# Performance work log

Measured on AMD Instinct MI355X. Metric: run time of the kernel, lower is better.

The kernel has to match this reference:

```python
import jax, jax.numpy as jnp
import numpy as np

VOCAB = 50000
OOV = 100
UNITS = 512
EMB = UNITS // 2
N_SENT = 32
N_WORDS = 50
B = 64


def setup_inputs() -> dict:
    key = jax.random.key(0)
    ks = jax.random.split(key, 16)
    g = lambda k, sh, s=0.02: (jax.random.normal(k, sh, dtype=jnp.float32) * s)
    inp = {
        "embedded_target": jax.random.normal(ks[0], (B, 1, EMB), dtype=jnp.float32),
        "hidden_dec": jax.random.normal(ks[1], (B, UNITS), dtype=jnp.float32),
        "encoded_sentences": jax.random.normal(ks[2], (B, N_SENT, UNITS), dtype=jnp.float32),
        "encoded_words": jax.random.normal(ks[3], (B, N_SENT, N_WORDS, UNITS), dtype=jnp.float32),
        "numeric_input": jax.random.randint(ks[4], (B, N_SENT * N_WORDS), 0, VOCAB + OOV),
        "batch_size": B,
        # GRU params (keras reset_after=True layout: 3 gates z,r,h stacked)
        "gru_Wx": g(ks[5], (EMB, 3 * UNITS)),
        "gru_Wh": g(ks[6], (UNITS, 3 * UNITS)),
        "gru_b": jnp.zeros((2, 3 * UNITS), dtype=jnp.float32),
        # attention params
        "W_att_sent": g(ks[7], (UNITS, UNITS)),
        "W_att_word": g(ks[8], (UNITS, UNITS)),
        # output projection (input is dec_units//2 after weight_dec)
        "fc_W": g(ks[9], (UNITS // 2, VOCAB)),
        "fc_b": jnp.zeros((VOCAB,), dtype=jnp.float32),
        "weight_context": g(ks[10], (UNITS, 1)),
        "weight_hidden": g(ks[11], (UNITS, 1)),
        "weight_dec": g(ks[12], (2 * UNITS, UNITS // 2)),
        "weight_input": g(ks[13], (UNITS // 2, 1)),
    }
    return inp


def _gru_step(x, h, Wx, Wh, b):
    # keras GRU cell, reset_after=True
    xm = x @ Wx + b[0]            # [B, 3U]
    hm = h @ Wh + b[1]            # [B, 3U]
    xz, xr, xh = jnp.split(xm, 3, axis=-1)
    hz, hr, hh = jnp.split(hm, 3, axis=-1)
    z = jax.nn.sigmoid(xz + hz)
    r = jax.nn.sigmoid(xr + hr)
    hcand = jnp.tanh(xh + r * hh)
    return z * h + (1.0 - z) * hcand


def reference(embedded_target, hidden_dec, encoded_sentences, encoded_words,
              gru_Wx, gru_Wh, gru_b, W_att_sent, W_att_word, fc_W, fc_b,
              weight_context, weight_hidden, weight_dec, weight_input,
              numeric_input, batch_size):
    # ---- GRU over the (length-1) target step; return last hidden ----
    def step(h, x_t):
        h2 = _gru_step(x_t, h, gru_Wx, gru_Wh, gru_b)
        return h2, None
    dec_output, _ = jax.lax.scan(step, hidden_dec, jnp.swapaxes(embedded_target, 0, 1))

    # ---- Luong (general) attention over sentences ----
    q = dec_output @ W_att_sent                              # [B, U]
    score_s = jnp.einsum("bd,bsd->bs", q, encoded_sentences)  # [B, S]
    alpha = jax.nn.softmax(score_s, axis=-1)                  # [B, S]
    context = jnp.einsum("bs,bsd->bd", alpha, encoded_sentences)  # [B, U]

    # ---- generation distribution ----
    x = jnp.concatenate([context, dec_output], axis=-1)       # [B, 2U]
    hidden_t = jnp.tanh(x @ weight_dec)                       # [B, U/2]
    gen_distr = jax.nn.softmax(hidden_t @ fc_W + fc_b, axis=-1)
    gen_distr = jnp.pad(gen_distr, ((0, 0), (0, OOV)))        # [B, V+OOV]

    # ---- hierarchical word attention (word softmax per sentence, scaled by alpha) ----
    qw = dec_output @ W_att_word                              # [B, U]
    score_w = jnp.einsum("bd,bswd->bsw", qw, encoded_words)   # [B, S, W]
    word_attn = jax.nn.softmax(score_w, axis=-1)              # softmax over words
    beta = (alpha[:, :, None] * word_attn).reshape(batch_size, -1)  # [B, S*W]

    # ---- batched scatter-add copy distribution ----
    ext = VOCAB + OOV
    bidx = jnp.arange(batch_size)[:, None]
    copy_distr = jnp.zeros((batch_size, ext), dtype=beta.dtype).at[bidx, numeric_input].add(beta)

    # ---- generation gate ----
    res1 = context @ weight_context
    res2 = dec_output @ weight_hidden
    res3 = embedded_target.reshape(batch_size, EMB) @ weight_input
    p_gen = jax.nn.sigmoid(res1 + res2 + res3)                # [B, 1]

    return dec_output, gen_distr, copy_distr, p_gen
```

## Files before the change

### kernel.cpp

```cpp
#include <hip/hip_runtime.h>

#define VOCAB 50000
#define OOV   100
#define EXT   50100
#define UNITS 512
#define EMB   256
#define NS    32
#define NW    50
#define BATCH 64
#define NQ    8
#define BINS_PER ((EXT + NQ - 1) / NQ)

#define GKC   24
#define QKC   8
#define HKC   16
#define NCB   ((VOCAB + 63) / 64)

#define COPYB (NQ * BATCH)
#define FINB  ((BATCH * (EXT / 4) + 255) / 256)

using short8 = __attribute__((ext_vector_type(8))) short;
using f32x4  = __attribute__((ext_vector_type(4))) float;

__device__ __forceinline__ float sigmoidf_(float x) { return 1.f / (1.f + __expf(-x)); }

__device__ __forceinline__ unsigned short f2bf_(float x) {
  union { float f; unsigned u; } c; c.f = x;
  return (unsigned short)((c.u + 0x8000u) >> 16);
}

__device__ __forceinline__ void gload_lds16(const void* g, void* l) {
  __builtin_amdgcn_global_load_lds(
      (const __attribute__((address_space(1))) unsigned int*)g,
      (__attribute__((address_space(3))) unsigned int*)l, 16, 0, 0);
}

__global__ __launch_bounds__(256) void k_gru_part(
    const float* __restrict__ emb, const float* __restrict__ h0,
    const float* __restrict__ Wx, const float* __restrict__ Wh,
    float* __restrict__ gates)
{
  __shared__ float sv[32];
  const int kc = blockIdx.x, b = blockIdx.y, t = threadIdx.x, u0 = 2 * t;
  const int base = kc * 32;
  const bool isx = base < EMB;
  if (t < 32) sv[t] = isx ? emb[b * EMB + base + t] : h0[b * UNITS + base - EMB + t];
  __syncthreads();

  const float* W = isx ? (Wx + (size_t)base * 1536) : (Wh + (size_t)(base - EMB) * 1536);
  float azx = 0.f, azy = 0.f, arx = 0.f, ary = 0.f, ahx = 0.f, ahy = 0.f;
  for (int i = 0; i < 32; i += 4) {
    float2 wz[4], wr[4], wh[4];
#pragma unroll
    for (int j = 0; j < 4; ++j) {
      const float* row = W + (size_t)(i + j) * 1536;
      wz[j] = *(const float2*)(row + u0);
      wr[j] = *(const float2*)(row + 512 + u0);
      wh[j] = *(const float2*)(row + 1024 + u0);
    }
#pragma unroll
    for (int j = 0; j < 4; ++j) {
      const float v = sv[i + j];
      azx = fmaf(v, wz[j].x, azx); azy = fmaf(v, wz[j].y, azy);
      arx = fmaf(v, wr[j].x, arx); ary = fmaf(v, wr[j].y, ary);
      ahx = fmaf(v, wh[j].x, ahx); ahy = fmaf(v, wh[j].y, ahy);
    }
  }
  float* gb_ = gates + (size_t)b * 2048;
  atomicAdd(gb_ + u0, azx);           atomicAdd(gb_ + u0 + 1, azy);
  atomicAdd(gb_ + 512 + u0, arx);     atomicAdd(gb_ + 512 + u0 + 1, ary);
  const int ho = isx ? 1024 : 1536;
  atomicAdd(gb_ + ho + u0, ahx);      atomicAdd(gb_ + ho + u0 + 1, ahy);
}

__global__ __launch_bounds__(256) void k_gru_fin(
    const float* __restrict__ gates, const float* __restrict__ gb,
    const float* __restrict__ h0, const float* __restrict__ emb,
    const float* __restrict__ whid, const float* __restrict__ winp,
    float* __restrict__ ws_dec, float* __restrict__ out_dec,
    float* __restrict__ ws_pgen)
{
  __shared__ float sred[256];
  const int b = blockIdx.x, t = threadIdx.x, u0 = 2 * t;
  const float* g_ = gates + (size_t)b * 2048;
  const float2 az  = *(const float2*)(g_ + u0);
  const float2 ar  = *(const float2*)(g_ + 512 + u0);
  const float2 ahx = *(const float2*)(g_ + 1024 + u0);
  const float2 ahh = *(const float2*)(g_ + 1536 + u0);

  const float2 b0z = *(const float2*)(gb + u0);
  const float2 b0r = *(const float2*)(gb + 512 + u0);
  const float2 b0h = *(const float2*)(gb + 1024 + u0);
  const float2 b1z = *(const float2*)(gb + 1536 + u0);
  const float2 b1r = *(const float2*)(gb + 1536 + 512 + u0);
  const float2 b1h = *(const float2*)(gb + 1536 + 1024 + u0);
  const float2 hp  = *(const float2*)(h0 + b * UNITS + u0);

  const float z0 = sigmoidf_(az.x + b0z.x + b1z.x);
  const float z1 = sigmoidf_(az.y + b0z.y + b1z.y);
  const float r0 = sigmoidf_(ar.x + b0r.x + b1r.x);
  const float r1 = sigmoidf_(ar.y + b0r.y + b1r.y);
  const float c0 = tanhf(ahx.x + b0h.x + r0 * (ahh.x + b1h.x));
  const float c1 = tanhf(ahx.y + b0h.y + r1 * (ahh.y + b1h.y));
  const float n0 = z0 * hp.x + (1.f - z0) * c0;
  const float n1 = z1 * hp.y + (1.f - z1) * c1;
  ws_dec[b * UNITS + u0]      = n0;
  ws_dec[b * UNITS + u0 + 1]  = n1;
  out_dec[b * UNITS + u0]     = n0;
  out_dec[b * UNITS + u0 + 1] = n1;

  float p = n0 * whid[u0] + n1 * whid[u0 + 1];
  if (u0 < EMB) p += emb[b * EMB + u0] * winp[u0] + emb[b * EMB + u0 + 1] * winp[u0 + 1];
  sred[t] = p;
  __syncthreads();
  for (int off = 128; off > 0; off >>= 1) {
    if (t < off) sred[t] += sred[t + off];
    __syncthreads();
  }
  if (t == 0) atomicAdd(ws_pgen + b, sred[0]);
}

__global__ __launch_bounds__(256) void k_qq(
    const float* __restrict__ ws_dec, const float* __restrict__ Wsent,
    const float* __restrict__ Wword, float* __restrict__ qsum)
{
  __shared__ float sdec[64];
  const int kc = blockIdx.x, b = blockIdx.y, t = threadIdx.x, u0 = 2 * t;
  const int k0 = kc * 64;
  if (t < 64) sdec[t] = ws_dec[b * UNITS + k0 + t];
  __syncthreads();

  float qx = 0.f, qy = 0.f, wx = 0.f, wy = 0.f;
  for (int i = 0; i < 64; i += 4) {
    float2 a[4], c[4];
#pragma unroll
    for (int j = 0; j < 4; ++j) {
      a[j] = *(const float2*)(Wsent + (size_t)(k0 + i + j) * UNITS + u0);
      c[j] = *(const float2*)(Wword + (size_t)(k0 + i + j) * UNITS + u0);
    }
#pragma unroll
    for (int j = 0; j < 4; ++j) {
      const float d = sdec[i + j];
      qx = fmaf(d, a[j].x, qx); qy = fmaf(d, a[j].y, qy);
      wx = fmaf(d, c[j].x, wx); wy = fmaf(d, c[j].y, wy);
    }
  }
  float* o = qsum + (size_t)b * 1024;
  atomicAdd(o + u0, qx);           atomicAdd(o + u0 + 1, qy);
  atomicAdd(o + 512 + u0, wx);     atomicAdd(o + 512 + u0 + 1, wy);
}

__global__ __launch_bounds__(512) void k_attn(
    const float* __restrict__ qsum, const float* __restrict__ encS,
    const float* __restrict__ wctx, float* __restrict__ ws_alpha,
    float* __restrict__ ctxsum, float* __restrict__ ws_pgen)
{
  __shared__ float sq[UNITS];
  __shared__ float sscore[NS];
  __shared__ float salpha[NS];
  __shared__ float sred[512];
  const int b = blockIdx.x, t = threadIdx.x;
  sq[t] = qsum[(size_t)b * 1024 + t];
  __syncthreads();

  const int wave = t >> 6, lane = t & 63;
  float qr[8];
#pragma unroll
  for (int j = 0; j < 8; ++j) qr[j] = sq[lane * 8 + j];
  for (int s = wave; s < NS; s += 8) {
    const float* base = encS + ((size_t)(b * NS + s)) * UNITS + lane * 8;
    const float4 v0 = *(const float4*)(base);
    const float4 v1 = *(const float4*)(base + 4);
    float acc = 0.f;
    acc = fmaf(v0.x, qr[0], acc); acc = fmaf(v0.y, qr[1], acc);
    acc = fmaf(v0.z, qr[2], acc); acc = fmaf(v0.w, qr[3], acc);
    acc = fmaf(v1.x, qr[4], acc); acc = fmaf(v1.y, qr[5], acc);
    acc = fmaf(v1.z, qr[6], acc); acc = fmaf(v1.w, qr[7], acc);
#pragma unroll
    for (int off = 32; off > 0; off >>= 1) acc += __shfl_down(acc, off);
    if (lane == 0) sscore[s] = acc;
  }
  __syncthreads();

  if (t < 32) {
    const float v = sscore[t];
    float m = v;
#pragma unroll
    for (int off = 16; off > 0; off >>= 1) m = fmaxf(m, __shfl_xor(m, off));
    const float e = __expf(v - m);
    float ssum = e;
#pragma unroll
    for (int off = 16; off > 0; off >>= 1) ssum += __shfl_xor(ssum, off);
    const float a = e / ssum;
    salpha[t] = a;
    ws_alpha[b * NS + t] = a;
  }
  __syncthreads();

  float c = 0.f;
#pragma unroll 4
  for (int s = 0; s < NS; ++s)
    c = fmaf(salpha[s], encS[((size_t)(b * NS + s)) * UNITS + t], c);
  ctxsum[b * UNITS + t] = c;

  float p = c * wctx[t];
  sred[t] = p;
  __syncthreads();
  for (int off = 256; off > 0; off >>= 1) {
    if (t < off) sred[t] += sred[t + off];
    __syncthreads();
  }
  if (t == 0) atomicAdd(ws_pgen + b, sred[0]);
}

__global__ __launch_bounds__(128) void k_ht(
    const float* __restrict__ ctxsum, const float* __restrict__ ws_dec,
    const float* __restrict__ wdec, float* __restrict__ htsum)
{
  __shared__ float scat[64];
  const int kc = blockIdx.x, b = blockIdx.y, t = threadIdx.x, u0 = 2 * t;
  const int k0 = kc * 64;
  if (t < 64) {
    const int k = k0 + t;
    scat[t] = (k < UNITS) ? ctxsum[b * UNITS + k] : ws_dec[b * UNITS + k - UNITS];
  }
  __syncthreads();

  float ax = 0.f, ay = 0.f;
  for (int i = 0; i < 64; i += 8) {
    float2 w[8];
#pragma unroll
    for (int j = 0; j < 8; ++j)
      w[j] = *(const float2*)(wdec + (size_t)(k0 + i + j) * 256 + u0);
#pragma unroll
    for (int j = 0; j < 8; ++j) {
      const float v = scat[i + j];
      ax = fmaf(v, w[j].x, ax); ay = fmaf(v, w[j].y, ay);
    }
  }
  atomicAdd(htsum + b * EMB + u0, ax);
  atomicAdd(htsum + b * EMB + u0 + 1, ay);
}

__global__ __launch_bounds__(256) void k_ht_fin(
    const float* __restrict__ htsum, const float* __restrict__ ws_pgen,
    unsigned short* __restrict__ Af, float* __restrict__ out_pgen)
{
  const int rb = blockIdx.x, t = threadIdx.x, l = t & 63, kh = t >> 6;
  const int row = rb * 16 + (l & 15);
#pragma unroll
  for (int ks = kh; ks < 8; ks += 4) {
    const int k0 = ks * 32 + (l >> 4) * 8;
    const float4 h0 = *(const float4*)(htsum + row * EMB + k0);
    const float4 h1 = *(const float4*)(htsum + row * EMB + k0 + 4);
    short8 v;
    v[0] = (short)f2bf_(tanhf(h0.x)); v[1] = (short)f2bf_(tanhf(h0.y));
    v[2] = (short)f2bf_(tanhf(h0.z)); v[3] = (short)f2bf_(tanhf(h0.w));
    v[4] = (short)f2bf_(tanhf(h1.x)); v[5] = (short)f2bf_(tanhf(h1.y));
    v[6] = (short)f2bf_(tanhf(h1.z)); v[7] = (short)f2bf_(tanhf(h1.w));
    *(short8*)(Af + ((size_t)(rb * 8 + ks)) * 512 + l * 8) = v;
  }
  if (rb == 0 && t < BATCH) out_pgen[t] = sigmoidf_(ws_pgen[t]);
}

__global__ __launch_bounds__(256, 2) void k_fc(
    const unsigned short* __restrict__ Af, const float* __restrict__ fcW,
    const float* __restrict__ fcb, float* __restrict__ out_gen,
    float* __restrict__ ws_rowsum)
{
  __shared__ float swt[256 * 64];
  const int cb = blockIdx.x;
  const int t = threadIdx.x, rb = t >> 6, l = t & 63;

  {
    const int c4 = l & 15;
    const int gc = cb * 64 + c4 * 4;
    const bool oob = (gc >= VOCAB);
    const int kr = rb * 64 + (l >> 4);
#pragma unroll
    for (int q = 0; q < 16; ++q) {
      const float* src = oob ? (fcW + c4 * 4)
                             : (fcW + (size_t)(kr + q * 4) * VOCAB + gc);
      gload_lds16(src, swt + rb * 4096 + q * 256);
    }
  }

  short8 a[8];
#pragma unroll
  for (int ks = 0; ks < 8; ++ks)
    a[ks] = *(const short8*)(Af + ((size_t)(rb * 8 + ks)) * 512 + l * 8);

  __syncthreads();

  f32x4 acc0 = {0.f, 0.f, 0.f, 0.f};
  f32x4 acc1 = {0.f, 0.f, 0.f, 0.f};
  f32x4 acc2 = {0.f, 0.f, 0.f, 0.f};
  f32x4 acc3 = {0.f, 0.f, 0.f, 0.f};

  const int cr = l & 15;
  const int kb = (l >> 4) * 8;
#pragma unroll
  for (int ks = 0; ks < 8; ++ks) {
    const float* kbase = swt + (size_t)(ks * 32 + kb) * 64 + cr;
    short8 b0, b1, b2, b3;
#pragma unroll
    for (int j = 0; j < 8; ++j) {
      const float* rowp = kbase + j * 64;
      b0[j] = (short)f2bf_(rowp[0]);
      b1[j] = (short)f2bf_(rowp[16]);
      b2[j] = (short)f2bf_(rowp[32]);
      b3[j] = (short)f2bf_(rowp[48]);
    }
    acc0 = __builtin_amdgcn_mfma_f32_16x16x32_bf16(a[ks], b0, acc0, 0, 0, 0);
    acc1 = __builtin_amdgcn_mfma_f32_16x16x32_bf16(a[ks], b1, acc1, 0, 0, 0);
    acc2 = __builtin_amdgcn_mfma_f32_16x16x32_bf16(a[ks], b2, acc2, 0, 0, 0);
    acc3 = __builtin_amdgcn_mfma_f32_16x16x32_bf16(a[ks], b3, acc3, 0, 0, 0);
  }

  const int colbase = cb * 64 + (l & 15);
  const int rowbase = rb * 16 + (l >> 4) * 4;
#pragma unroll
  for (int p = 0; p < 4; ++p) {
    float rs = 0.f;
    const float av[4] = {acc0[p], acc1[p], acc2[p], acc3[p]};
#pragma unroll
    for (int f = 0; f < 4; ++f) {
      const int col = colbase + f * 16;
      if (col < VOCAB) {
        const float e = __expf(av[f] + fcb[col]);
        out_gen[(size_t)(rowbase + p) * EXT + col] = e;
        rs += e;
      }
    }
    rs += __shfl_xor(rs, 1); rs += __shfl_xor(rs, 2);
    rs += __shfl_xor(rs, 4); rs += __shfl_xor(rs, 8);
    if ((l & 15) == 0) atomicAdd(ws_rowsum + rowbase + p, rs);
  }
}

__global__ __launch_bounds__(256) void k_word(
    const float* __restrict__ qsum, const float* __restrict__ encW,
    const float* __restrict__ ws_alpha, float* __restrict__ ws_beta)
{
  __shared__ float sqw[UNITS];
  __shared__ float sscore[64];
  const int bi = blockIdx.x;
  const int b = bi >> 5, s = bi & 31;
  const int t = threadIdx.x;
  sqw[t]       = qsum[(size_t)b * 1024 + 512 + t];
  sqw[t + 256] = qsum[(size_t)b * 1024 + 768 + t];
  __syncthreads();

  const int wave = t >> 6, lane = t & 63;
  float qr[8];
#pragma unroll
  for (int j = 0; j < 8; ++j) qr[j] = sqw[lane * 8 + j];
  const float* base = encW + ((size_t)(b * NS + s)) * NW * UNITS + lane * 8;

#pragma unroll
  for (int i = 0; i < 4; ++i) {
    const int r0 = i * 16 + wave * 4;
    if (r0 >= NW) break;
    float a0 = 0.f, a1 = 0.f, a2 = 0.f, a3 = 0.f;
    {
      const float* row = base + (size_t)r0 * UNITS;
      const float4 v0 = *(const float4*)(row);
      const float4 v1 = *(const float4*)(row + 4);
      a0 = v0.x*qr[0] + v0.y*qr[1] + v0.z*qr[2] + v0.w*qr[3]
         + v1.x*qr[4] + v1.y*qr[5] + v1.z*qr[6] + v1.w*qr[7];
    }
    if (r0 + 1 < NW) {
      const float* row = base + (size_t)(r0 + 1) * UNITS;
      const float4 v0 = *(const float4*)(row);
      const float4 v1 = *(const float4*)(row + 4);
      a1 = v0.x*qr[0] + v0.y*qr[1] + v0.z*qr[2] + v0.w*qr[3]
         + v1.x*qr[4] + v1.y*qr[5] + v1.z*qr[6] + v1.w*qr[7];
    }
    if (r0 + 2 < NW) {
      const float* row = base + (size_t)(r0 + 2) * UNITS;
      const float4 v0 = *(const float4*)(row);
      const float4 v1 = *(const float4*)(row + 4);
      a2 = v0.x*qr[0] + v0.y*qr[1] + v0.z*qr[2] + v0.w*qr[3]
         + v1.x*qr[4] + v1.y*qr[5] + v1.z*qr[6] + v1.w*qr[7];
    }
    if (r0 + 3 < NW) {
      const float* row = base + (size_t)(r0 + 3) * UNITS;
      const float4 v0 = *(const float4*)(row);
      const float4 v1 = *(const float4*)(row + 4);
      a3 = v0.x*qr[0] + v0.y*qr[1] + v0.z*qr[2] + v0.w*qr[3]
         + v1.x*qr[4] + v1.y*qr[5] + v1.z*qr[6] + v1.w*qr[7];
    }
#pragma unroll
    for (int off = 32; off > 0; off >>= 1) {
      a0 += __shfl_xor(a0, off);
      a1 += __shfl_xor(a1, off);
      a2 += __shfl_xor(a2, off);
      a3 += __shfl_xor(a3, off);
    }
    if (lane == 0) {
      sscore[r0] = a0;
      if (r0 + 1 < NW) sscore[r0 + 1] = a1;
      if (r0 + 2 < NW) sscore[r0 + 2] = a2;
      if (r0 + 3 < NW) sscore[r0 + 3] = a3;
    }
  }
  __syncthreads();

  if (t < 64) {
    const float v = (t < NW) ? sscore[t] : -1e30f;
    float m = v;
#pragma unroll
    for (int off = 32; off > 0; off >>= 1) m = fmaxf(m, __shfl_xor(m, off));
    const float e = (t < NW) ? __expf(v - m) : 0.f;
    float sum = e;
#pragma unroll
    for (int off = 32; off > 0; off >>= 1) sum += __shfl_xor(sum, off);
    if (t < NW)
      ws_beta[b * (NS * NW) + s * NW + t] = ws_alpha[b * NS + s] * e / sum;
  }
}

__global__ __launch_bounds__(256) void k_tail(
    const int* __restrict__ nidx, const float* __restrict__ ws_beta,
    const float* __restrict__ ws_rowsum, float* __restrict__ out_copy,
    float* __restrict__ out_gen)
{
  __shared__ float shist[BINS_PER];
  const int bid = blockIdx.x, t = threadIdx.x;
  if (bid < COPYB) {
    const int q = bid & (NQ - 1), b = bid >> 3;
    const int base = q * BINS_PER;
    const int len = min(BINS_PER, EXT - base);

    for (int j = t; j < BINS_PER; j += 256) shist[j] = 0.f;
    __syncthreads();

    for (int e = t; e < NS * NW; e += 256) {
      const int rel = nidx[b * (NS * NW) + e] - base;
      if (rel >= 0 && rel < len) atomicAdd(shist + rel, ws_beta[b * (NS * NW) + e]);
    }
    __syncthreads();

    for (int j = t; j < len; j += 256)
      out_copy[(size_t)b * EXT + base + j] = shist[j];
  } else {
    const int i4 = (bid - COPYB) * 256 + t;
    if (i4 < BATCH * (EXT / 4)) {
      const int b = i4 / (EXT / 4);
      const int c4 = (i4 - b * (EXT / 4)) * 4;
      float4 v = make_float4(0.f, 0.f, 0.f, 0.f);
      if (c4 < VOCAB) {
        v = *(const float4*)(out_gen + (size_t)b * EXT + c4);
        const float inv = 1.f / ws_rowsum[b];
        v.x *= inv; v.y *= inv; v.z *= inv; v.w *= inv;
      }
      *(float4*)(out_gen + (size_t)b * EXT + c4) = v;
    }
  }
}

extern "C" void kernel_launch(void* const* d_in, const int* in_sizes, int n_in,
                              void* d_out, int out_size, void* d_ws, size_t ws_size,
                              hipStream_t stream)
{
  const float* emb   = (const float*)d_in[0];
  const float* h0    = (const float*)d_in[1];
  const float* encS  = (const float*)d_in[2];
  const float* encW  = (const float*)d_in[3];
  const int*   nidx  = (const int*)d_in[4];
  const float* Wx    = (const float*)d_in[6];
  const float* Wh    = (const float*)d_in[7];
  const float* gb    = (const float*)d_in[8];
  const float* Wsent = (const float*)d_in[9];
  const float* Wword = (const float*)d_in[10];
  const float* fcW   = (const float*)d_in[11];
  const float* fcb   = (const float*)d_in[12];
  const float* wctx  = (const float*)d_in[13];
  const float* whid  = (const float*)d_in[14];
  const float* wdec  = (const float*)d_in[15];
  const float* winp  = (const float*)d_in[16];

  float* ws = (float*)d_ws;
  float* ws_gates  = ws;
  float* ws_qsum   = ws_gates + BATCH * 2048;
  float* ws_ctxsum = ws_qsum + BATCH * 1024;
  float* ws_htsum  = ws_ctxsum + BATCH * UNITS;
  float* ws_rowsum = ws_htsum + BATCH * EMB;
  float* ws_pgen   = ws_rowsum + BATCH;
  const size_t zfloats = (size_t)BATCH * (2048 + 1024 + 512 + 256) + 2 * BATCH;
  float* ws_dec    = ws_pgen + BATCH;
  float* ws_alpha  = ws_dec + BATCH * UNITS;
  float* ws_beta   = ws_alpha + BATCH * NS;
  unsigned short* ws_af = (unsigned short*)(ws_beta + BATCH * NS * NW);

  float* out      = (float*)d_out;
  float* out_dec  = out;
  float* out_gen  = out + BATCH * UNITS;
  float* out_copy = out_gen + (size_t)BATCH * EXT;
  float* out_pgen = out_copy + (size_t)BATCH * EXT;

  hipMemsetAsync(ws, 0, zfloats * sizeof(float), stream);

  k_gru_part<<<dim3(GKC, BATCH), 256, 0, stream>>>(emb, h0, Wx, Wh, ws_gates);
  k_gru_fin<<<BATCH, 256, 0, stream>>>(ws_gates, gb, h0, emb, whid, winp,
                                       ws_dec, out_dec, ws_pgen);
  k_qq<<<dim3(QKC, BATCH), 256, 0, stream>>>(ws_dec, Wsent, Wword, ws_qsum);
  k_attn<<<BATCH, 512, 0, stream>>>(ws_qsum, encS, wctx, ws_alpha,
                                    ws_ctxsum, ws_pgen);
  k_ht<<<dim3(HKC, BATCH), 128, 0, stream>>>(ws_ctxsum, ws_dec, wdec, ws_htsum);
  k_ht_fin<<<4, 256, 0, stream>>>(ws_htsum, ws_pgen, ws_af, out_pgen);
  k_fc<<<NCB, 256, 0, stream>>>(ws_af, fcW, fcb, out_gen, ws_rowsum);
  k_word<<<BATCH * NS, 256, 0, stream>>>(ws_qsum, encW, ws_alpha, ws_beta);
  k_tail<<<COPYB + FINB, 256, 0, stream>>>(nidx, ws_beta, ws_rowsum,
                                           out_copy, out_gen);
}
```

Baseline: 505.0 us.

## Fuse kernel chain with last-block atomic tickets and merge word-attn with fc

Cuts the launch chain from nine kernels to five. Each split-K partial kernel (GRU, q-projection, weight_dec) now takes an atomic ticket per batch or globally, and the last-arriving block performs the finalize step (gate nonlinearity, attention softmax/context, tanh+bf16 pack) that used to be a separate launch. The word-attention blocks and the fc MFMA blocks share one launch, and the fc path stages its weight tile in two halves so it uses 32KB of LDS instead of 64KB, allowing more resident blocks. The aim is to remove launch gaps and tail idle time, at the cost of threadfence and atomic-counter overhead and serial finalize work done by one block.

```diff
diff --git a/kernel.cpp b/kernel.cpp
--- a/kernel.cpp
+++ b/kernel.cpp
@@ -15,6 +15,7 @@
 #define QKC   8
 #define HKC   16
 #define NCB   ((VOCAB + 63) / 64)
+#define WORDB (BATCH * NS)
 
 #define COPYB (NQ * BATCH)
 #define FINB  ((BATCH * (EXT / 4) + 255) / 256)
@@ -35,12 +36,18 @@
       (__attribute__((address_space(3))) unsigned int*)l, 16, 0, 0);
 }
 
-__global__ __launch_bounds__(256) void k_gru_part(
+__global__ __launch_bounds__(256) void k_gru(
     const float* __restrict__ emb, const float* __restrict__ h0,
     const float* __restrict__ Wx, const float* __restrict__ Wh,
-    float* __restrict__ gates)
+    const float* __restrict__ gb, const float* __restrict__ whid,
+    const float* __restrict__ winp,
+    float* __restrict__ gates, float* __restrict__ ws_dec,
+    float* __restrict__ out_dec, float* __restrict__ ws_pgen,
+    unsigned* __restrict__ cnt)
 {
   __shared__ float sv[32];
+  __shared__ float sred[256];
+  __shared__ unsigned sticket;
   const int kc = blockIdx.x, b = blockIdx.y, t = threadIdx.x, u0 = 2 * t;
   const int base = kc * 32;
   const bool isx = base < EMB;
@@ -48,7 +55,7 @@
   __syncthreads();
 
   const float* W = isx ? (Wx + (size_t)base * 1536) : (Wh + (size_t)(base - EMB) * 1536);
-  float azx = 0.f, azy = 0.f, arx = 0.f, ary = 0.f, ahx = 0.f, ahy = 0.f;
+  float azx = 0.f, azy = 0.f, arx = 0.f, ary = 0.f, ahxx = 0.f, ahy = 0.f;
   for (int i = 0; i < 32; i += 4) {
     float2 wz[4], wr[4], wh[4];
 #pragma unroll
@@ -63,25 +70,22 @@
       const float v = sv[i + j];
       azx = fmaf(v, wz[j].x, azx); azy = fmaf(v, wz[j].y, azy);
       arx = fmaf(v, wr[j].x, arx); ary = fmaf(v, wr[j].y, ary);
-      ahx = fmaf(v, wh[j].x, ahx); ahy = fmaf(v, wh[j].y, ahy);
+      ahxx = fmaf(v, wh[j].x, ahxx); ahy = fmaf(v, wh[j].y, ahy);
     }
   }
   float* gb_ = gates + (size_t)b * 2048;
   atomicAdd(gb_ + u0, azx);           atomicAdd(gb_ + u0 + 1, azy);
   atomicAdd(gb_ + 512 + u0, arx);     atomicAdd(gb_ + 512 + u0 + 1, ary);
   const int ho = isx ? 1024 : 1536;
-  atomicAdd(gb_ + ho + u0, ahx);      atomicAdd(gb_ + ho + u0 + 1, ahy);
-}
-
-__global__ __launch_bounds__(256) void k_gru_fin(
-    const float* __restrict__ gates, const float* __restrict__ gb,
-    const float* __restrict__ h0, const float* __restrict__ emb,
-    const float* __restrict__ whid, const float* __restrict__ winp,
-    float* __restrict__ ws_dec, float* __restrict__ out_dec,
-    float* __restrict__ ws_pgen)
-{
-  __shared__ float sred[256];
-  const int b = blockIdx.x, t = threadIdx.x, u0 = 2 * t;
+  atomicAdd(gb_ + ho + u0, ahxx);     atomicAdd(gb_ + ho + u0 + 1, ahy);
+
+  __threadfence();
+  __syncthreads();
+  if (t == 0) sticket = atomicAdd(&cnt[b], 1u);
+  __syncthreads();
+  if (sticket != GKC - 1) return;
+  __threadfence();
+
   const float* g_ = gates + (size_t)b * 2048;
   const float2 az  = *(const float2*)(g_ + u0);
   const float2 ar  = *(const float2*)(g_ + 512 + u0);
@@ -120,11 +124,19 @@
   if (t == 0) atomicAdd(ws_pgen + b, sred[0]);
 }
 
-__global__ __launch_bounds__(256) void k_qq(
+__global__ __launch_bounds__(256) void k_qa(
     const float* __restrict__ ws_dec, const float* __restrict__ Wsent,
-    const float* __restrict__ Wword, float* __restrict__ qsum)
+    const float* __restrict__ Wword, const float* __restrict__ encS,
+    const float* __restrict__ wctx,
+    float* __restrict__ qsum, float* __restrict__ ws_alpha,
+    float* __restrict__ ctxsum, float* __restrict__ ws_pgen,
+    unsigned* __restrict__ cnt)
 {
   __shared__ float sdec[64];
+  __shared__ float sq[UNITS];
+  __shared__ float sscore[NS], salpha[NS];
+  __shared__ float sred[256];
+  __shared__ unsigned sticket;
   const int kc = blockIdx.x, b = blockIdx.y, t = threadIdx.x, u0 = 2 * t;
   const int k0 = kc * 64;
   if (t < 64) sdec[t] = ws_dec[b * UNITS + k0 + t];
@@ -148,26 +160,23 @@
   float* o = qsum + (size_t)b * 1024;
   atomicAdd(o + u0, qx);           atomicAdd(o + u0 + 1, qy);
   atomicAdd(o + 512 + u0, wx);     atomicAdd(o + 512 + u0 + 1, wy);
-}
-
-__global__ __launch_bounds__(512) void k_attn(
-    const float* __restrict__ qsum, const float* __restrict__ encS,
-    const float* __restrict__ wctx, float* __restrict__ ws_alpha,
-    float* __restrict__ ctxsum, float* __restrict__ ws_pgen)
-{
-  __shared__ float sq[UNITS];
-  __shared__ float sscore[NS];
-  __shared__ float salpha[NS];
-  __shared__ float sred[512];
-  const int b = blockIdx.x, t = threadIdx.x;
-  sq[t] = qsum[(size_t)b * 1024 + t];
+
+  __threadfence();
+  __syncthreads();
+  if (t == 0) sticket = atomicAdd(&cnt[b], 1u);
+  __syncthreads();
+  if (sticket != QKC - 1) return;
+  __threadfence();
+
+  sq[t]       = o[t];
+  sq[t + 256] = o[t + 256];
   __syncthreads();
 
   const int wave = t >> 6, lane = t & 63;
   float qr[8];
 #pragma unroll
   for (int j = 0; j < 8; ++j) qr[j] = sq[lane * 8 + j];
-  for (int s = wave; s < NS; s += 8) {
+  for (int s = wave; s < NS; s += 4) {
     const float* base = encS + ((size_t)(b * NS + s)) * UNITS + lane * 8;
     const float4 v0 = *(const float4*)(base);
     const float4 v1 = *(const float4*)(base + 4);
@@ -197,27 +206,33 @@
   }
   __syncthreads();
 
-  float c = 0.f;
+  float c0 = 0.f, c1 = 0.f;
 #pragma unroll 4
-  for (int s = 0; s < NS; ++s)
-    c = fmaf(salpha[s], encS[((size_t)(b * NS + s)) * UNITS + t], c);
-  ctxsum[b * UNITS + t] = c;
-
-  float p = c * wctx[t];
-  sred[t] = p;
-  __syncthreads();
-  for (int off = 256; off > 0; off >>= 1) {
+  for (int s = 0; s < NS; ++s) {
+    const float* es = encS + ((size_t)(b * NS + s)) * UNITS;
+    c0 = fmaf(salpha[s], es[t], c0);
+    c1 = fmaf(salpha[s], es[t + 256], c1);
+  }
+  ctxsum[b * UNITS + t]       = c0;
+  ctxsum[b * UNITS + t + 256] = c1;
+
+  sred[t] = c0 * wctx[t] + c1 * wctx[t + 256];
+  __syncthreads();
+  for (int off = 128; off > 0; off >>= 1) {
     if (t < off) sred[t] += sred[t + off];
     __syncthreads();
   }
   if (t == 0) atomicAdd(ws_pgen + b, sred[0]);
 }
 
-__global__ __launch_bounds__(128) void k_ht(
+__global__ __launch_bounds__(128) void k_hta(
     const float* __restrict__ ctxsum, const float* __restrict__ ws_dec,
-    const float* __restrict__ wdec, float* __restrict__ htsum)
+    const float* __restrict__ wdec, const float* __restrict__ ws_pgen,
+    float* __restrict__ htsum, unsigned short* __restrict__ Af,
+    float* __restrict__ out_pgen, unsigned* __restrict__ cnt)
 {
   __shared__ float scat[64];
+  __shared__ unsigned sticket;
   const int kc = blockIdx.x, b = blockIdx.y, t = threadIdx.x, u0 = 2 * t;
   const int k0 = kc * 64;
   if (t < 64) {
@@ -240,57 +255,129 @@
   }
   atomicAdd(htsum + b * EMB + u0, ax);
   atomicAdd(htsum + b * EMB + u0 + 1, ay);
-}
-
-__global__ __launch_bounds__(256) void k_ht_fin(
-    const float* __restrict__ htsum, const float* __restrict__ ws_pgen,
-    unsigned short* __restrict__ Af, float* __restrict__ out_pgen)
+
+  __threadfence();
+  __syncthreads();
+  if (t == 0) sticket = atomicAdd(cnt, 1u);
+  __syncthreads();
+  if (sticket != HKC * BATCH - 1) return;
+  __threadfence();
+
+  const int l = t & 63, wv = t >> 6;
+#pragma unroll
+  for (int rb = 0; rb < 4; ++rb) {
+    for (int ks = wv; ks < 8; ks += 2) {
+      const int row = rb * 16 + (l & 15);
+      const int kk = ks * 32 + (l >> 4) * 8;
+      const float4 h0v = *(const float4*)(htsum + row * EMB + kk);
+      const float4 h1v = *(const float4*)(htsum + row * EMB + kk + 4);
+      short8 v;
+      v[0] = (short)f2bf_(tanhf(h0v.x)); v[1] = (short)f2bf_(tanhf(h0v.y));
+      v[2] = (short)f2bf_(tanhf(h0v.z)); v[3] = (short)f2bf_(tanhf(h0v.w));
+      v[4] = (short)f2bf_(tanhf(h1v.x)); v[5] = (short)f2bf_(tanhf(h1v.y));
+      v[6] = (short)f2bf_(tanhf(h1v.z)); v[7] = (short)f2bf_(tanhf(h1v.w));
+      *(short8*)(Af + ((size_t)(rb * 8 + ks)) * 512 + l * 8) = v;
+    }
+  }
+  if (t < BATCH) out_pgen[t] = sigmoidf_(ws_pgen[t]);
+}
+
+__global__ __launch_bounds__(256, 5) void k_fw(
+    const unsigned short* __restrict__ Af, const float* __restrict__ fcW,
+    const float* __restrict__ fcb, const float* __restrict__ qsum,
+    const float* __restrict__ encW, const float* __restrict__ ws_alpha,
+    float* __restrict__ out_gen, float* __restrict__ ws_rowsum,
+    float* __restrict__ ws_beta)
 {
-  const int rb = blockIdx.x, t = threadIdx.x, l = t & 63, kh = t >> 6;
-  const int row = rb * 16 + (l & 15);
-#pragma unroll
-  for (int ks = kh; ks < 8; ks += 4) {
-    const int k0 = ks * 32 + (l >> 4) * 8;
-    const float4 h0 = *(const float4*)(htsum + row * EMB + k0);
-    const float4 h1 = *(const float4*)(htsum + row * EMB + k0 + 4);
-    short8 v;
-    v[0] = (short)f2bf_(tanhf(h0.x)); v[1] = (short)f2bf_(tanhf(h0.y));
-    v[2] = (short)f2bf_(tanhf(h0.z)); v[3] = (short)f2bf_(tanhf(h0.w));
-    v[4] = (short)f2bf_(tanhf(h1.x)); v[5] = (short)f2bf_(tanhf(h1.y));
-    v[6] = (short)f2bf_(tanhf(h1.z)); v[7] = (short)f2bf_(tanhf(h1.w));
-    *(short8*)(Af + ((size_t)(rb * 8 + ks)) * 512 + l * 8) = v;
-  }
-  if (rb == 0 && t < BATCH) out_pgen[t] = sigmoidf_(ws_pgen[t]);
-}
-
-__global__ __launch_bounds__(256, 2) void k_fc(
-    const unsigned short* __restrict__ Af, const float* __restrict__ fcW,
-    const float* __restrict__ fcb, float* __restrict__ out_gen,
-    float* __restrict__ ws_rowsum)
-{
-  __shared__ float swt[256 * 64];
-  const int cb = blockIdx.x;
-  const int t = threadIdx.x, rb = t >> 6, l = t & 63;
-
-  {
-    const int c4 = l & 15;
-    const int gc = cb * 64 + c4 * 4;
-    const bool oob = (gc >= VOCAB);
-    const int kr = rb * 64 + (l >> 4);
-#pragma unroll
-    for (int q = 0; q < 16; ++q) {
-      const float* src = oob ? (fcW + c4 * 4)
-                             : (fcW + (size_t)(kr + q * 4) * VOCAB + gc);
-      gload_lds16(src, swt + rb * 4096 + q * 256);
-    }
-  }
+  __shared__ __align__(16) float smem[8192];
+  const int bid = blockIdx.x, t = threadIdx.x;
+
+  if (bid < WORDB) {
+    float* sqw    = smem;
+    float* sscore = smem + 512;
+    const int b = bid >> 5, s = bid & 31;
+    sqw[t]       = qsum[(size_t)b * 1024 + 512 + t];
+    sqw[t + 256] = qsum[(size_t)b * 1024 + 768 + t];
+    __syncthreads();
+
+    const int wave = t >> 6, lane = t & 63;
+    float qr[8];
+#pragma unroll
+    for (int j = 0; j < 8; ++j) qr[j] = sqw[lane * 8 + j];
+    const float* base = encW + ((size_t)(b * NS + s)) * NW * UNITS + lane * 8;
+
+#pragma unroll
+    for (int i = 0; i < 4; ++i) {
+      const int r0 = i * 16 + wave * 4;
+      if (r0 >= NW) break;
+      float a0 = 0.f, a1 = 0.f, a2 = 0.f, a3 = 0.f;
+      {
+        const float* row = base + (size_t)r0 * UNITS;
+        const float4 v0 = *(const float4*)(row);
+        const float4 v1 = *(const float4*)(row + 4);
+        a0 = v0.x*qr[0] + v0.y*qr[1] + v0.z*qr[2] + v0.w*qr[3]
+           + v1.x*qr[4] + v1.y*qr[5] + v1.z*qr[6] + v1.w*qr[7];
+      }
+      if (r0 + 1 < NW) {
+        const float* row = base + (size_t)(r0 + 1) * UNITS;
+        const float4 v0 = *(const float4*)(row);
+        const float4 v1 = *(const float4*)(row + 4);
+        a1 = v0.x*qr[0] + v0.y*qr[1] + v0.z*qr[2] + v0.w*qr[3]
+           + v1.x*qr[4] + v1.y*qr[5] + v1.z*qr[6] + v1.w*qr[7];
+      }
+      if (r0 + 2 < NW) {
+        const float* row = base + (size_t)(r0 + 2) * UNITS;
+        const float4 v0 = *(const float4*)(row);
+        const float4 v1 = *(const float4*)(row + 4);
+        a2 = v0.x*qr[0] + v0.y*qr[1] + v0.z*qr[2] + v0.w*qr[3]
+           + v1.x*qr[4] + v1.y*qr[5] + v1.z*qr[6] + v1.w*qr[7];
+      }
+      if (r0 + 3 < NW) {
+        const float* row = base + (size_t)(r0 + 3) * UNITS;
+        const float4 v0 = *(const float4*)(row);
+        const float4 v1 = *(const float4*)(row + 4);
+        a3 = v0.x*qr[0] + v0.y*qr[1] + v0.z*qr[2] + v0.w*qr[3]
+           + v1.x*qr[4] + v1.y*qr[5] + v1.z*qr[6] + v1.w*qr[7];
+      }
+#pragma unroll
+      for (int off = 32; off > 0; off >>= 1) {
+        a0 += __shfl_xor(a0, off);
+        a1 += __shfl_xor(a1, off);
+        a2 += __shfl_xor(a2, off);
+        a3 += __shfl_xor(a3, off);
+      }
+      if (lane == 0) {
+        sscore[r0] = a0;
+        if (r0 + 1 < NW) sscore[r0 + 1] = a1;
+        if (r0 + 2 < NW) sscore[r0 + 2] = a2;
+        if (r0 + 3 < NW) sscore[r0 + 3] = a3;
+      }
+    }
+    __syncthreads();
+
+    if (t < 64) {
+      const float v = (t < NW) ? sscore[t] : -1e30f;
+      float m = v;
+#pragma unroll
+      for (int off = 32; off > 0; off >>= 1) m = fmaxf(m, __shfl_xor(m, off));
+      const float e = (t < NW) ? __expf(v - m) : 0.f;
+      float sum = e;
+#pragma unroll
+      for (int off = 32; off > 0; off >>= 1) sum += __shfl_xor(sum, off);
+      if (t < NW)
+        ws_beta[b * (NS * NW) + s * NW + t] = ws_alpha[b * NS + s] * e / sum;
+    }
+    return;
+  }
+
+  const int cb = bid - WORDB;
+  float* swt = smem;
+  const int rb = t >> 6, l = t & 63;
 
   short8 a[8];
 #pragma unroll
   for (int ks = 0; ks < 8; ++ks)
     a[ks] = *(const short8*)(Af + ((size_t)(rb * 8 + ks)) * 512 + l * 8);
-
-  __syncthreads();
 
   f32x4 acc0 = {0.f, 0.f, 0.f, 0.f};
   f32x4 acc1 = {0.f, 0.f, 0.f, 0.f};
@@ -299,22 +386,39 @@
 
   const int cr = l & 15;
   const int kb = (l >> 4) * 8;
-#pragma unroll
-  for (int ks = 0; ks < 8; ++ks) {
-    const float* kbase = swt + (size_t)(ks * 32 + kb) * 64 + cr;
-    short8 b0, b1, b2, b3;
-#pragma unroll
-    for (int j = 0; j < 8; ++j) {
-      const float* rowp = kbase + j * 64;
-      b0[j] = (short)f2bf_(rowp[0]);
-      b1[j] = (short)f2bf_(rowp[16]);
-      b2[j] = (short)f2bf_(rowp[32]);
-      b3[j] = (short)f2bf_(rowp[48]);
-    }
-    acc0 = __builtin_amdgcn_mfma_f32_16x16x32_bf16(a[ks], b0, acc0, 0, 0, 0);
-    acc1 = __builtin_amdgcn_mfma_f32_16x16x32_bf16(a[ks], b1, acc1, 0, 0, 0);
-    acc2 = __builtin_amdgcn_mfma_f32_16x16x32_bf16(a[ks], b2, acc2, 0, 0, 0);
-    acc3 = __builtin_amdgcn_mfma_f32_16x16x32_bf16(a[ks], b3, acc3, 0, 0, 0);
+  const int gc = cb * 64 + cr * 4;
+  const bool oob = (gc >= VOCAB);
+
+#pragma unroll
+  for (int h = 0; h < 2; ++h) {
+    if (h) __syncthreads();
+    const int krow0 = h * 128 + rb * 32;
+#pragma unroll
+    for (int q = 0; q < 8; ++q) {
+      const float* src = oob ? (fcW + cr * 4)
+          : (fcW + (size_t)(krow0 + q * 4 + (l >> 4)) * VOCAB + gc);
+      gload_lds16(src, swt + (rb * 32 + q * 4) * 64);
+    }
+    __syncthreads();
+
+#pragma unroll
+    for (int ks2 = 0; ks2 < 4; ++ks2) {
+      const float* kbase = swt + (size_t)(ks2 * 32 + kb) * 64 + cr;
+      short8 b0, b1, b2, b3;
+#pragma unroll
+      for (int j = 0; j < 8; ++j) {
+        const float* rowp = kbase + j * 64;
+        b0[j] = (short)f2bf_(rowp[0]);
+        b1[j] = (short)f2bf_(rowp[16]);
+        b2[j] = (short)f2bf_(rowp[32]);
+        b3[j] = (short)f2bf_(rowp[48]);
+      }
+      const int ks = h * 4 + ks2;
+      acc0 = __builtin_amdgcn_mfma_f32_16x16x32_bf16(a[ks], b0, acc0, 0, 0, 0);
+      acc1 = __builtin_amdgcn_mfma_f32_16x16x32_bf16(a[ks], b1, acc1, 0, 0, 0);
+      acc2 = __builtin_amdgcn_mfma_f32_16x16x32_bf16(a[ks], b2, acc2, 0, 0, 0);
+      acc3 = __builtin_amdgcn_mfma_f32_16x16x32_bf16(a[ks], b3, acc3, 0, 0, 0);
+    }
   }
 
   const int colbase = cb * 64 + (l & 15);
@@ -335,88 +439,6 @@
     rs += __shfl_xor(rs, 1); rs += __shfl_xor(rs, 2);
     rs += __shfl_xor(rs, 4); rs += __shfl_xor(rs, 8);
     if ((l & 15) == 0) atomicAdd(ws_rowsum + rowbase + p, rs);
-  }
-}
-
-__global__ __launch_bounds__(256) void k_word(
-    const float* __restrict__ qsum, const float* __restrict__ encW,
-    const float* __restrict__ ws_alpha, float* __restrict__ ws_beta)
-{
-  __shared__ float sqw[UNITS];
-  __shared__ float sscore[64];
-  const int bi = blockIdx.x;
-  const int b = bi >> 5, s = bi & 31;
-  const int t = threadIdx.x;
-  sqw[t]       = qsum[(size_t)b * 1024 + 512 + t];
-  sqw[t + 256] = qsum[(size_t)b * 1024 + 768 + t];
-  __syncthreads();
-
-  const int wave = t >> 6, lane = t & 63;
-  float qr[8];
-#pragma unroll
-  for (int j = 0; j < 8; ++j) qr[j] = sqw[lane * 8 + j];
-  const float* base = encW + ((size_t)(b * NS + s)) * NW * UNITS + lane * 8;
-
-#pragma unroll
-  for (int i = 0; i < 4; ++i) {
-    const int r0 = i * 16 + wave * 4;
-    if (r0 >= NW) break;
-    float a0 = 0.f, a1 = 0.f, a2 = 0.f, a3 = 0.f;
-    {
-      const float* row = base + (size_t)r0 * UNITS;
-      const float4 v0 = *(const float4*)(row);
-      const float4 v1 = *(const float4*)(row + 4);
-      a0 = v0.x*qr[0] + v0.y*qr[1] + v0.z*qr[2] + v0.w*qr[3]
-         + v1.x*qr[4] + v1.y*qr[5] + v1.z*qr[6] + v1.w*qr[7];
-    }
-    if (r0 + 1 < NW) {
-      const float* row = base + (size_t)(r0 + 1) * UNITS;
-      const float4 v0 = *(const float4*)(row);
-      const float4 v1 = *(const float4*)(row + 4);
-      a1 = v0.x*qr[0] + v0.y*qr[1] + v0.z*qr[2] + v0.w*qr[3]
-         + v1.x*qr[4] + v1.y*qr[5] + v1.z*qr[6] + v1.w*qr[7];
-    }
-    if (r0 + 2 < NW) {
-      const float* row = base + (size_t)(r0 + 2) * UNITS;
-      const float4 v0 = *(const float4*)(row);
-      const float4 v1 = *(const float4*)(row + 4);
-      a2 = v0.x*qr[0] + v0.y*qr[1] + v0.z*qr[2] + v0.w*qr[3]
-         + v1.x*qr[4] + v1.y*qr[5] + v1.z*qr[6] + v1.w*qr[7];
-    }
-    if (r0 + 3 < NW) {
-      const float* row = base + (size_t)(r0 + 3) * UNITS;
-      const float4 v0 = *(const float4*)(row);
-      const float4 v1 = *(const float4*)(row + 4);
-      a3 = v0.x*qr[0] + v0.y*qr[1] + v0.z*qr[2] + v0.w*qr[3]
-         + v1.x*qr[4] + v1.y*qr[5] + v1.z*qr[6] + v1.w*qr[7];
-    }
-#pragma unroll
-    for (int off = 32; off > 0; off >>= 1) {
-      a0 += __shfl_xor(a0, off);
-      a1 += __shfl_xor(a1, off);
-      a2 += __shfl_xor(a2, off);
-      a3 += __shfl_xor(a3, off);
-    }
-    if (lane == 0) {
-      sscore[r0] = a0;
-      if (r0 + 1 < NW) sscore[r0 + 1] = a1;
-      if (r0 + 2 < NW) sscore[r0 + 2] = a2;
-      if (r0 + 3 < NW) sscore[r0 + 3] = a3;
-    }
-  }
-  __syncthreads();
-
-  if (t < 64) {
-    const float v = (t < NW) ? sscore[t] : -1e30f;
-    float m = v;
-#pragma unroll
-    for (int off = 32; off > 0; off >>= 1) m = fmaxf(m, __shfl_xor(m, off));
-    const float e = (t < NW) ? __expf(v - m) : 0.f;
-    float sum = e;
-#pragma unroll
-    for (int off = 32; off > 0; off >>= 1) sum += __shfl_xor(sum, off);
-    if (t < NW)
-      ws_beta[b * (NS * NW) + s * NW + t] = ws_alpha[b * NS + s] * e / sum;
   }
 }
 
@@ -487,8 +509,9 @@
   float* ws_htsum  = ws_ctxsum + BATCH * UNITS;
   float* ws_rowsum = ws_htsum + BATCH * EMB;
   float* ws_pgen   = ws_rowsum + BATCH;
-  const size_t zfloats = (size_t)BATCH * (2048 + 1024 + 512 + 256) + 2 * BATCH;
-  float* ws_dec    = ws_pgen + BATCH;
+  unsigned* ws_cnt = (unsigned*)(ws_pgen + BATCH);
+  const size_t zfloats = (size_t)BATCH * (2048 + 1024 + 512 + 256) + 2 * BATCH + 192;
+  float* ws_dec    = (float*)(ws_cnt + 192);
   float* ws_alpha  = ws_dec + BATCH * UNITS;
   float* ws_beta   = ws_alpha + BATCH * NS;
   unsigned short* ws_af = (unsigned short*)(ws_beta + BATCH * NS * NW);
@@ -501,16 +524,17 @@
 
   hipMemsetAsync(ws, 0, zfloats * sizeof(float), stream);
 
-  k_gru_part<<<dim3(GKC, BATCH), 256, 0, stream>>>(emb, h0, Wx, Wh, ws_gates);
-  k_gru_fin<<<BATCH, 256, 0, stream>>>(ws_gates, gb, h0, emb, whid, winp,
-                                       ws_dec, out_dec, ws_pgen);
-  k_qq<<<dim3(QKC, BATCH), 256, 0, stream>>>(ws_dec, Wsent, Wword, ws_qsum);
-  k_attn<<<BATCH, 512, 0, stream>>>(ws_qsum, encS, wctx, ws_alpha,
-                                    ws_ctxsum, ws_pgen);
-  k_ht<<<dim3(HKC, BATCH), 128, 0, stream>>>(ws_ctxsum, ws_dec, wdec, ws_htsum);
-  k_ht_fin<<<4, 256, 0, stream>>>(ws_htsum, ws_pgen, ws_af, out_pgen);
-  k_fc<<<NCB, 256, 0, stream>>>(ws_af, fcW, fcb, out_gen, ws_rowsum);
-  k_word<<<BATCH * NS, 256, 0, stream>>>(ws_qsum, encW, ws_alpha, ws_beta);
+  k_gru<<<dim3(GKC, BATCH), 256, 0, stream>>>(emb, h0, Wx, Wh, gb, whid, winp,
+                                              ws_gates, ws_dec, out_dec,
+                                              ws_pgen, ws_cnt);
+  k_qa<<<dim3(QKC, BATCH), 256, 0, stream>>>(ws_dec, Wsent, Wword, encS, wctx,
+                                             ws_qsum, ws_alpha, ws_ctxsum,
+                                             ws_pgen, ws_cnt + 64);
+  k_hta<<<dim3(HKC, BATCH), 128, 0, stream>>>(ws_ctxsum, ws_dec, wdec, ws_pgen,
+                                              ws_htsum, ws_af, out_pgen,
+                                              ws_cnt + 128);
+  k_fw<<<WORDB + NCB, 256, 0, stream>>>(ws_af, fcW, fcb, ws_qsum, encW,
+                                        ws_alpha, out_gen, ws_rowsum, ws_beta);
   k_tail<<<COPYB + FINB, 256, 0, stream>>>(nidx, ws_beta, ws_rowsum,
                                            out_copy, out_gen);
 }
```

Measured after the change: 721.2 us. 42.8% more time.
